# Kernel tuning notes

Hardware: AMD Instinct MI355X
Metric: run time of the kernel (lower is better)

The kernel has to match this reference:

```python
import jax, jax.numpy as jnp
import numpy as np

K = 7
TAU = 0.1
ANCHORS = 512
CANDIDATES = 2048
B, C, H, W = 16, 384, 96, 96
RADIUS = K // 2
K2 = K * K

_dy, _dx = np.meshgrid(np.arange(-RADIUS, RADIUS + 1), np.arange(-RADIUS, RADIUS + 1), indexing='ij')
OFF_Y = jnp.asarray(_dy.reshape(-1).astype(np.int32))  # [K2]
OFF_X = jnp.asarray(_dx.reshape(-1).astype(np.int32))  # [K2]


def _normalize(x):
    # F.normalize(x, dim=1): L2 over channel dim, eps=1e-12
    n = jnp.sqrt(jnp.sum(x * x, axis=1, keepdims=True))
    return x / jnp.maximum(n, 1e-12)


def _local_sims_shared(feat, anchors_yx):
    # feat [B,C,H,W], anchors_yx [M,2] shared across batch -> [B,M,K2]
    ys, xs = anchors_yx[:, 0], anchors_yx[:, 1]          # [M]
    yy = ys[:, None] + OFF_Y[None, :]                    # [M,K2]
    xx = xs[:, None] + OFF_X[None, :]                    # [M,K2]
    center = feat[:, :, ys, xs]                          # [B,C,M]
    neigh = feat[:, :, yy, xx]                           # [B,C,M,K2]
    return jnp.einsum('bcm,bcmk->bmk', center, neigh)


def _local_sims_per_image(feat, anchors_byx):
    # feat [B,C,H,W], anchors_byx [Bm,M,2] per-image anchors -> [B,M,K2]
    b, c, h, w = feat.shape
    flat = feat.reshape(b, c, h * w)
    ys, xs = anchors_byx[..., 0], anchors_byx[..., 1]    # [B,M]
    lin_c = ys * w + xs                                  # [B,M]
    lin_n = (ys[..., None] + OFF_Y) * w + (xs[..., None] + OFF_X)  # [B,M,K2]
    gather = jax.vmap(lambda f, idx: f[:, idx])          # f [C,HW], idx [...]
    center = gather(flat, lin_c)                         # [B,C,M]
    neigh = gather(flat, lin_n)                          # [B,C,M,K2]
    return jnp.einsum('bcm,bcmk->bmk', center, neigh)


def setup_inputs() -> dict:
    key = jax.random.key(0)
    k1, k2, k3, k4 = jax.random.split(key, 4)
    student = jax.random.normal(k1, (B, C, H, W), dtype=jnp.float32)
    teacher = jax.random.normal(k2, (B, C, H, W), dtype=jnp.float32)
    # anchors valid region: [radius, H-radius-1] x [radius, W-radius-1]
    ys = jax.random.randint(k3, (CANDIDATES,), RADIUS, H - RADIUS, dtype=jnp.int32)
    xs = jax.random.randint(k4, (CANDIDATES,), RADIUS, W - RADIUS, dtype=jnp.int32)
    candidate_anchors = jnp.stack([ys, xs], axis=1)      # [Mc,2]
    return {"student": student, "teacher": teacher, "candidate_anchors": candidate_anchors}


def reference(student, teacher, candidate_anchors):
    t_norm = _normalize(teacher)
    # --- teacher-entropy based anchor selection (no_grad in original) ---
    sim_cand = _local_sims_shared(t_norm, candidate_anchors) / TAU   # [B,Mc,K2]
    p = jax.nn.softmax(sim_cand, axis=2)
    ent = -jnp.sum(p * jnp.log(p + 1e-6), axis=2)                    # [B,Mc]
    # per_image=True, kcenter_top_m=0 -> lowest-entropy top-k per image
    _, sel_idx = jax.lax.top_k(-ent, ANCHORS)                        # [B,A]
    anchors = candidate_anchors[sel_idx]                             # [B,A,2]
    # --- local affinity KL ---
    s_norm = _normalize(student)
    sim_s = _local_sims_per_image(s_norm, anchors) / TAU             # [B,A,K2]
    sim_t = _local_sims_per_image(t_norm, anchors) / TAU
    log_ps = jax.nn.log_softmax(sim_s, axis=2)
    log_pt = jax.nn.log_softmax(sim_t, axis=2)
    pt = jnp.exp(log_pt)
    # F.kl_div(log_ps, pt, 'none').sum(2).mean()
    loss = jnp.mean(jnp.sum(pt * (log_pt - log_ps), axis=2))
    return loss
```

## Files before the change

kernel.cpp:

```cpp
#include <hip/hip_runtime.h>
#include <math.h>

#define B 16
#define C 384
#define CPAD 385
#define H 96
#define W 96
#define HW (H*W)
#define M 2048
#define K2 49
#define RAD 3
#define NSEL 512
#define INV_TAU 10.0f
#define TP 32

__device__ inline float wave_max(float v){
  #pragma unroll
  for (int o = 32; o; o >>= 1) v = fmaxf(v, __shfl_xor(v, o));
  return v;
}
__device__ inline float wave_sum(float v){
  #pragma unroll
  for (int o = 32; o; o >>= 1) v += __shfl_xor(v, o);
  return v;
}

__device__ __forceinline__ float patch_sims(const float* __restrict__ img,
                                            int ay, int ax, int lane){
  int g = lane >> 4, t = lane & 15;
  const float2* cp = (const float2*)(img + (size_t)(ay * W + ax) * C) + t;
  float2 c[12];
  #pragma unroll
  for (int j = 0; j < 12; ++j) c[j] = cp[16 * j];
  float mysim = 0.f;
  float2 bA[12], bB[12];

#define PLOAD(buf, pp) { \
    int dxl = ((pp) & 1) * 4 + g; if (dxl > 6) dxl = 6; \
    const float2* np = (const float2*)(img + \
        (size_t)((ay + ((pp) >> 1) - RAD) * W + (ax - RAD + dxl)) * C) + t; \
    _Pragma("unroll") for (int j = 0; j < 12; ++j) buf[j] = np[16 * j]; }

#define PCOMP(buf, pp) { \
    float a0 = 0.f, a1 = 0.f; \
    _Pragma("unroll") for (int j = 0; j < 6; ++j){ \
      a0 = fmaf(c[j].x, buf[j].x, a0); a0 = fmaf(c[j].y, buf[j].y, a0); \
      a1 = fmaf(c[j+6].x, buf[j+6].x, a1); a1 = fmaf(c[j+6].y, buf[j+6].y, a1); } \
    float a = a0 + a1; \
    a += __shfl_xor(a, 8); a += __shfl_xor(a, 4); \
    a += __shfl_xor(a, 2); a += __shfl_xor(a, 1); \
    int kbase = ((pp) >> 1) * 7 + ((pp) & 1) * 4; \
    int npass = ((pp) & 1) ? 3 : 4; \
    float v = __shfl(a, ((lane - kbase) & 3) << 4); \
    if (lane >= kbase && lane < kbase + npass) mysim = v; }

  PLOAD(bA, 0);
  #pragma unroll
  for (int pp = 0; pp < 14; pp += 2){
    PLOAD(bB, pp + 1);
    __builtin_amdgcn_sched_barrier(0);
    PCOMP(bA, pp);
    if (pp + 2 < 14) PLOAD(bA, pp + 2);
    __builtin_amdgcn_sched_barrier(0);
    PCOMP(bB, pp + 1);
  }
#undef PLOAD
#undef PCOMP
  return mysim;
}


__global__ void tnorm_kernel(const float* __restrict__ src, float* __restrict__ dst){
  int blk = blockIdx.x;
  int b = blk / (HW / TP);
  int pixbase = (blk % (HW / TP)) * TP;
  __shared__ float tile[TP][CPAD];
  __shared__ float scale[TP];
  const float* sb = src + (size_t)b * C * HW + pixbase;
  int tx = threadIdx.x & 31;
  int ty = threadIdx.x >> 5;
  #pragma unroll 4
  for (int c0 = 0; c0 < C; c0 += 8){
    tile[tx][c0 + ty] = sb[(size_t)(c0 + ty) * HW + tx];
  }
  __syncthreads();
  int pix = threadIdx.x >> 3;
  int j = threadIdx.x & 7;
  float ss = 0.f;
  #pragma unroll 4
  for (int c = j * 48; c < j * 48 + 48; ++c){ float v = tile[pix][c]; ss = fmaf(v, v, ss); }
  ss += __shfl_xor(ss, 1); ss += __shfl_xor(ss, 2); ss += __shfl_xor(ss, 4);
  if (j == 0) scale[pix] = 1.0f / fmaxf(sqrtf(ss), 1e-12f);
  __syncthreads();
  float4* db4 = (float4*)(dst + ((size_t)b * HW + pixbase) * C);
  #pragma unroll 4
  for (int l = threadIdx.x; l < TP * (C / 4); l += 256){
    int p = l / (C / 4), c4 = l - p * (C / 4);
    float s = scale[p];
    float4 v;
    v.x = tile[p][c4 * 4 + 0] * s;
    v.y = tile[p][c4 * 4 + 1] * s;
    v.z = tile[p][c4 * 4 + 2] * s;
    v.w = tile[p][c4 * 4 + 3] * s;
    db4[(size_t)p * (C / 4) + c4] = v;
  }
}

__global__ void sort_kernel(const int* __restrict__ anch, int* __restrict__ order){
  int i = blockIdx.x * 256 + threadIdx.x;
  __shared__ int keys[M];
  for (int j = threadIdx.x; j < M; j += 256){
    int ay = anch[2 * j], ax = anch[2 * j + 1];
    keys[j] = (((ay >> 3) * 12 + (ax >> 3)) << 11) + j;
  }
  __syncthreads();
  int ki = keys[i];
  int r = 0;
  #pragma unroll 4
  for (int j = 0; j < M; ++j) r += (keys[j] < ki) ? 1 : 0;
  order[r] = i;
}

__global__ __launch_bounds__(256, 4) void cand2_kernel(const float* __restrict__ fT,
                             const int* __restrict__ anch, const int* __restrict__ order,
                             float* __restrict__ simc, float* __restrict__ ent){
  int nwg = B * M / 4;
  int bid = blockIdx.x;
  int swz = (bid & 7) * (nwg >> 3) + (bid >> 3);
  int bm = swz * 4 + (threadIdx.x >> 6);
  int b = bm >> 11, mi = bm & (M - 1);
  int lane = threadIdx.x & 63;
  int m = order ? order[mi] : mi;
  int ay = anch[2 * m], ax = anch[2 * m + 1];
  const float* img = fT + (size_t)b * HW * C;
  float mysim = patch_sims(img, ay, ax, lane) * INV_TAU;

  float v = (lane < K2) ? mysim : -INFINITY;
  float mx = wave_max(v);
  float e = (lane < K2) ? expf(mysim - mx) : 0.f;
  float se = wave_sum(e);
  float p = e / se;
  float term = (lane < K2) ? (-p * logf(p + 1e-6f)) : 0.f;
  float en = wave_sum(term);
  size_t slot = (size_t)b * M + m;
  if (lane == 0) ent[slot] = en;
  if (lane < K2) simc[slot * K2 + lane] = mysim;
}

__global__ void select_kernel(const float* __restrict__ ent, int* __restrict__ sel){
  int blk = blockIdx.x;
  int b = blk >> 3;
  int i = (blk & 7) * 256 + threadIdx.x;
  __shared__ float se[M];
  for (int j = threadIdx.x; j < M; j += 256) se[j] = ent[b * M + j];
  __syncthreads();
  float ei = se[i];
  int r = 0;
  for (int j = 0; j < M; ++j){
    float ej = se[j];
    r += (ej < ei) || (ej == ei && j < i);
  }
  if (r < NSEL) sel[b * NSEL + r] = i;
}

__global__ __launch_bounds__(256, 4) void kl2_kernel(const float* __restrict__ fS,
                           const int* __restrict__ anch,
                           const float* __restrict__ simc, const int* __restrict__ sel,
                           float* __restrict__ klpart){
  int bj = blockIdx.x * 4 + (threadIdx.x >> 6);
  int b = bj >> 9, j = bj & (NSEL - 1);
  int lane = threadIdx.x & 63;
  int m = sel[b * NSEL + j];
  int ay = anch[2 * m], ax = anch[2 * m + 1];
  const float* img = fS + (size_t)b * HW * C;
  float sim_sv = patch_sims(img, ay, ax, lane) * INV_TAU;
  float sim_tv = (lane < K2) ? simc[((size_t)b * M + m) * K2 + lane] : -INFINITY;

  float vs = (lane < K2) ? sim_sv : -INFINITY;
  float mxs = wave_max(vs);
  float es = (lane < K2) ? expf(sim_sv - mxs) : 0.f;
  float sums = wave_sum(es);
  float ls = sim_sv - mxs - logf(sums);

  float mxt = wave_max(sim_tv);
  float et = (lane < K2) ? expf(sim_tv - mxt) : 0.f;
  float sumt = wave_sum(et);
  float lt = sim_tv - mxt - logf(sumt);

  float pt = et / sumt;
  float term = (lane < K2) ? pt * (lt - ls) : 0.f;
  float kl = wave_sum(term);
  if (lane == 0) klpart[bj] = kl;
}

__global__ void reduce_kernel(const float* __restrict__ part, float* __restrict__ out){
  float s = 0.f;
  for (int i = threadIdx.x; i < B * NSEL; i += 256) s += part[i];
  s = wave_sum(s);
  __shared__ float wsum[4];
  if ((threadIdx.x & 63) == 0) wsum[threadIdx.x >> 6] = s;
  __syncthreads();
  if (threadIdx.x == 0) out[0] = (wsum[0] + wsum[1] + wsum[2] + wsum[3]) * (1.0f / (B * NSEL));
}


__global__ void norms_kernel(const float* __restrict__ t, const float* __restrict__ s,
                             float* __restrict__ inv_t, float* __restrict__ inv_s){
  int pix = blockIdx.x * blockDim.x + threadIdx.x;
  if (pix >= B * HW) return;
  int b = pix / HW, p = pix - b * HW;
  const float* tb = t + (size_t)b * C * HW + p;
  const float* sb = s + (size_t)b * C * HW + p;
  float at = 0.f, as = 0.f;
  #pragma unroll 4
  for (int c = 0; c < C; ++c){
    float v = tb[(size_t)c * HW]; at = fmaf(v, v, at);
    float u = sb[(size_t)c * HW]; as = fmaf(u, u, as);
  }
  inv_t[pix] = 1.0f / fmaxf(sqrtf(at), 1e-12f);
  inv_s[pix] = 1.0f / fmaxf(sqrtf(as), 1e-12f);
}

__global__ void cand_kernel(const float* __restrict__ t, const int* __restrict__ anch,
                            const float* __restrict__ inv_t,
                            float* __restrict__ simc, float* __restrict__ ent){
  int bm = blockIdx.x;
  int b = bm >> 11, m = bm & (M - 1);
  int lane = threadIdx.x;
  int ay = anch[2 * m], ax = anch[2 * m + 1];
  int k = lane < K2 ? lane : 0;
  int dy = k / 7 - RAD, dx = k - (k / 7) * 7 - RAD;
  int pc = ay * W + ax;
  int pk = (ay + dy) * W + (ax + dx);
  const float* base = t + (size_t)b * C * HW;
  float acc = 0.f;
  #pragma unroll 4
  for (int c = 0; c < C; ++c){
    const float* row = base + (size_t)c * HW;
    acc = fmaf(row[pc], row[pk], acc);
  }
  float sim = acc * inv_t[b * HW + pc] * inv_t[b * HW + pk] * INV_TAU;
  float v = (lane < K2) ? sim : -INFINITY;
  float mx = wave_max(v);
  float e = (lane < K2) ? expf(sim - mx) : 0.f;
  float se = wave_sum(e);
  float p = e / se;
  float term = (lane < K2) ? (-p * logf(p + 1e-6f)) : 0.f;
  float en = wave_sum(term);
  if (lane == 0) ent[bm] = en;
  if (lane < K2) simc[(size_t)bm * K2 + lane] = sim;
}

__global__ void kl_kernel(const float* __restrict__ s, const int* __restrict__ anch,
                          const float* __restrict__ inv_s, const float* __restrict__ simc,
                          const int* __restrict__ sel, float* __restrict__ klpart){
  int bj = blockIdx.x;
  int b = bj >> 9, j = bj & (NSEL - 1);
  int lane = threadIdx.x;
  int m = sel[b * NSEL + j];
  int ay = anch[2 * m], ax = anch[2 * m + 1];
  int k = lane < K2 ? lane : 0;
  int dy = k / 7 - RAD, dx = k - (k / 7) * 7 - RAD;
  int pc = ay * W + ax;
  int pk = (ay + dy) * W + (ax + dx);
  const float* base = s + (size_t)b * C * HW;
  float acc = 0.f;
  #pragma unroll 4
  for (int c = 0; c < C; ++c){
    const float* row = base + (size_t)c * HW;
    acc = fmaf(row[pc], row[pk], acc);
  }
  float sim_sv = acc * inv_s[b * HW + pc] * inv_s[b * HW + pk] * INV_TAU;
  float sim_tv = (lane < K2) ? simc[((size_t)b * M + m) * K2 + lane] : -INFINITY;

  float vs = (lane < K2) ? sim_sv : -INFINITY;
  float mxs = wave_max(vs);
  float es = (lane < K2) ? expf(sim_sv - mxs) : 0.f;
  float sums = wave_sum(es);
  float ls = sim_sv - mxs - logf(sums);

  float mxt = wave_max(sim_tv);
  float et = (lane < K2) ? expf(sim_tv - mxt) : 0.f;
  float sumt = wave_sum(et);
  float lt = sim_tv - mxt - logf(sumt);

  float pt = et / sumt;
  float term = (lane < K2) ? pt * (lt - ls) : 0.f;
  float kl = wave_sum(term);
  if (lane == 0) klpart[bj] = kl;
}

extern "C" void kernel_launch(void* const* d_in, const int* in_sizes, int n_in,
                              void* d_out, int out_size, void* d_ws, size_t ws_size,
                              hipStream_t stream){
  const float* student = (const float*)d_in[0];
  const float* teacher = (const float*)d_in[1];
  const int*   anch    = (const int*)d_in[2];
  float* out = (float*)d_out;

  const size_t fbuf_elems = (size_t)B * HW * C;
  const size_t simc_elems = (size_t)B * M * K2;
  size_t req_base = (fbuf_elems + simc_elems + (size_t)B * M + (size_t)B * NSEL) * sizeof(float)
                  + (size_t)B * NSEL * sizeof(int);
  size_t req_sort = req_base + (size_t)M * sizeof(int);

  if (ws_size >= req_base){
    float* fbuf   = (float*)d_ws;
    float* simc   = fbuf + fbuf_elems;
    float* ent    = simc + simc_elems;
    float* klpart = ent + (size_t)B * M;
    int*   sel    = (int*)(klpart + (size_t)B * NSEL);
    int*   order  = (ws_size >= req_sort) ? (sel + (size_t)B * NSEL) : (int*)nullptr;

    hipLaunchKernelGGL(tnorm_kernel, dim3(B * (HW / TP)), dim3(256), 0, stream, teacher, fbuf);
    if (order)
      hipLaunchKernelGGL(sort_kernel, dim3(8), dim3(256), 0, stream, anch, order);
    hipLaunchKernelGGL(cand2_kernel, dim3(B * M / 4), dim3(256), 0, stream, fbuf, anch, order, simc, ent);
    hipLaunchKernelGGL(select_kernel, dim3(B * 8), dim3(256), 0, stream, ent, sel);
    hipLaunchKernelGGL(tnorm_kernel, dim3(B * (HW / TP)), dim3(256), 0, stream, student, fbuf);
    hipLaunchKernelGGL(kl2_kernel, dim3(B * NSEL / 4), dim3(256), 0, stream, fbuf, anch, simc, sel, klpart);
    hipLaunchKernelGGL(reduce_kernel, dim3(1), dim3(256), 0, stream, klpart, out);
  } else {
    float* ws2    = (float*)d_ws;
    float* inv_t  = ws2;
    float* inv_s  = inv_t + B * HW;
    float* ent    = inv_s + B * HW;
    float* simc   = ent + B * M;
    float* klpart = simc + simc_elems;
    int*   sel    = (int*)(klpart + (size_t)B * NSEL);

    hipLaunchKernelGGL(norms_kernel, dim3((B * HW + 255) / 256), dim3(256), 0, stream,
                       teacher, student, inv_t, inv_s);
    hipLaunchKernelGGL(cand_kernel, dim3(B * M), dim3(64), 0, stream,
                       teacher, anch, inv_t, simc, ent);
    hipLaunchKernelGGL(select_kernel, dim3(B * 8), dim3(256), 0, stream, ent, sel);
    hipLaunchKernelGGL(kl_kernel, dim3(B * NSEL), dim3(64), 0, stream,
                       student, anch, inv_s, simc, sel, klpart);
    hipLaunchKernelGGL(reduce_kernel, dim3(1), dim3(256), 0, stream, klpart, out);
  }
}
```

Measured before the change: 911.5 us.

## Split normalize into norms pass plus chunked transpose-scale, sort selected anchors spatially

Replaces the single tnorm transpose kernel, which held a whole 32x384 tile in LDS, with a norms kernel that computes inverse norms for teacher and student together, plus a transpose-and-scale kernel that streams 96-channel chunks through a smaller LDS tile. Selected anchors are now sorted by spatial bucket per image so kl2 reads neighbouring patches with better cache locality, and kl2 gets a block swizzle. Both the cand2 and kl2 occupancy hints rise to 8 blocks. Inputs are now read an extra time for the norms pass, and the added selsort launch costs some time.

```diff
diff --git a/kernel.cpp b/kernel.cpp
--- a/kernel.cpp
+++ b/kernel.cpp
@@ -3,7 +3,6 @@
 
 #define B 16
 #define C 384
-#define CPAD 385
 #define H 96
 #define W 96
 #define HW (H*W)
@@ -12,7 +11,8 @@
 #define RAD 3
 #define NSEL 512
 #define INV_TAU 10.0f
-#define TP 32
+#define TSP 64
+#define CCH 96
 
 __device__ inline float wave_max(float v){
   #pragma unroll
@@ -70,39 +70,59 @@
 }
 
 
-__global__ void tnorm_kernel(const float* __restrict__ src, float* __restrict__ dst){
+__global__ void norms2_kernel(const float* __restrict__ t, const float* __restrict__ s,
+                              float* __restrict__ inv_t, float* __restrict__ inv_s){
+  int pix = blockIdx.x * 256 + threadIdx.x;
+  int b = pix / HW, p = pix - b * HW;
+  const float* tb = t + (size_t)b * C * HW + p;
+  const float* sb = s + (size_t)b * C * HW + p;
+  float pt[8], ps[8];
+  #pragma unroll
+  for (int k = 0; k < 8; ++k){
+    float at = 0.f, as = 0.f;
+    #pragma unroll 4
+    for (int c = k * 48; c < k * 48 + 48; ++c){
+      float v = tb[(size_t)c * HW]; at = fmaf(v, v, at);
+      float u = sb[(size_t)c * HW]; as = fmaf(u, u, as);
+    }
+    pt[k] = at; ps[k] = as;
+  }
+  float at = ((pt[0]+pt[1]) + (pt[2]+pt[3])) + ((pt[4]+pt[5]) + (pt[6]+pt[7]));
+  float as = ((ps[0]+ps[1]) + (ps[2]+ps[3])) + ((ps[4]+ps[5]) + (ps[6]+ps[7]));
+  inv_t[pix] = 1.0f / fmaxf(sqrtf(at), 1e-12f);
+  inv_s[pix] = 1.0f / fmaxf(sqrtf(as), 1e-12f);
+}
+
+__global__ __launch_bounds__(256) void tscale_kernel(const float* __restrict__ src,
+                              const float* __restrict__ inv, float* __restrict__ dst){
   int blk = blockIdx.x;
-  int b = blk / (HW / TP);
-  int pixbase = (blk % (HW / TP)) * TP;
-  __shared__ float tile[TP][CPAD];
-  __shared__ float scale[TP];
-  const float* sb = src + (size_t)b * C * HW + pixbase;
-  int tx = threadIdx.x & 31;
-  int ty = threadIdx.x >> 5;
-  #pragma unroll 4
-  for (int c0 = 0; c0 < C; c0 += 8){
-    tile[tx][c0 + ty] = sb[(size_t)(c0 + ty) * HW + tx];
-  }
-  __syncthreads();
-  int pix = threadIdx.x >> 3;
-  int j = threadIdx.x & 7;
-  float ss = 0.f;
-  #pragma unroll 4
-  for (int c = j * 48; c < j * 48 + 48; ++c){ float v = tile[pix][c]; ss = fmaf(v, v, ss); }
-  ss += __shfl_xor(ss, 1); ss += __shfl_xor(ss, 2); ss += __shfl_xor(ss, 4);
-  if (j == 0) scale[pix] = 1.0f / fmaxf(sqrtf(ss), 1e-12f);
-  __syncthreads();
-  float4* db4 = (float4*)(dst + ((size_t)b * HW + pixbase) * C);
-  #pragma unroll 4
-  for (int l = threadIdx.x; l < TP * (C / 4); l += 256){
-    int p = l / (C / 4), c4 = l - p * (C / 4);
-    float s = scale[p];
-    float4 v;
-    v.x = tile[p][c4 * 4 + 0] * s;
-    v.y = tile[p][c4 * 4 + 1] * s;
-    v.z = tile[p][c4 * 4 + 2] * s;
-    v.w = tile[p][c4 * 4 + 3] * s;
-    db4[(size_t)p * (C / 4) + c4] = v;
+  int b = blk / (HW / TSP);
+  int pixbase = (blk % (HW / TSP)) * TSP;
+  __shared__ float tile[TSP][CCH + 1];
+  int tx = threadIdx.x & 63;
+  int ty = threadIdx.x >> 6;
+  const float* sb = src + (size_t)b * C * HW + pixbase + tx;
+  float sc = inv[b * HW + pixbase + tx];
+  float* db = dst + ((size_t)b * HW + pixbase) * C;
+  #pragma unroll
+  for (int ch = 0; ch < C / CCH; ++ch){
+    #pragma unroll
+    for (int cc = 0; cc < CCH; cc += 4){
+      tile[tx][cc + ty] = sb[(size_t)(ch * CCH + cc + ty) * HW] * sc;
+    }
+    __syncthreads();
+    #pragma unroll
+    for (int j = 0; j < 6; ++j){
+      int idx = threadIdx.x + 256 * j;
+      int pix = idx / 24, c4 = idx - pix * 24;
+      float4 v;
+      v.x = tile[pix][c4 * 4 + 0];
+      v.y = tile[pix][c4 * 4 + 1];
+      v.z = tile[pix][c4 * 4 + 2];
+      v.w = tile[pix][c4 * 4 + 3];
+      ((float4*)(db + (size_t)pix * C + ch * CCH))[c4] = v;
+    }
+    __syncthreads();
   }
 }
 
@@ -121,7 +141,7 @@
   order[r] = i;
 }
 
-__global__ __launch_bounds__(256, 4) void cand2_kernel(const float* __restrict__ fT,
+__global__ __launch_bounds__(256, 8) void cand2_kernel(const float* __restrict__ fT,
                              const int* __restrict__ anch, const int* __restrict__ order,
                              float* __restrict__ simc, float* __restrict__ ent){
   int nwg = B * M / 4;
@@ -163,14 +183,39 @@
   if (r < NSEL) sel[b * NSEL + r] = i;
 }
 
-__global__ __launch_bounds__(256, 4) void kl2_kernel(const float* __restrict__ fS,
+__global__ void selsort_kernel(const int* __restrict__ anch, const int* __restrict__ sel,
+                               int* __restrict__ sel2){
+  int b = blockIdx.x;
+  __shared__ int keys[NSEL];
+  __shared__ int pos[NSEL];
+  for (int j = threadIdx.x; j < NSEL; j += 256){
+    int m = sel[b * NSEL + j];
+    int ay = anch[2 * m], ax = anch[2 * m + 1];
+    keys[j] = (((ay >> 3) * 12 + (ax >> 3)) << 11) | m;
+    pos[j] = j;
+  }
+  __syncthreads();
+  for (int j = threadIdx.x; j < NSEL; j += 256){
+    int kj = keys[j];
+    int r = 0;
+    #pragma unroll 4
+    for (int i = 0; i < NSEL; ++i) r += (keys[i] < kj) ? 1 : 0;
+    sel2[b * NSEL + r] = (pos[j] << 11) | (kj & (M - 1));
+  }
+}
+
+__global__ __launch_bounds__(256, 8) void kl2_kernel(const float* __restrict__ fS,
                            const int* __restrict__ anch,
-                           const float* __restrict__ simc, const int* __restrict__ sel,
+                           const float* __restrict__ simc, const int* __restrict__ sel2,
                            float* __restrict__ klpart){
-  int bj = blockIdx.x * 4 + (threadIdx.x >> 6);
+  int nwg = B * NSEL / 4;
+  int bid = blockIdx.x;
+  int swz = (bid & 7) * (nwg >> 3) + (bid >> 3);
+  int bj = swz * 4 + (threadIdx.x >> 6);
   int b = bj >> 9, j = bj & (NSEL - 1);
   int lane = threadIdx.x & 63;
-  int m = sel[b * NSEL + j];
+  int e2 = sel2[b * NSEL + j];
+  int m = e2 & (M - 1), pos = e2 >> 11;
   int ay = anch[2 * m], ax = anch[2 * m + 1];
   const float* img = fS + (size_t)b * HW * C;
   float sim_sv = patch_sims(img, ay, ax, lane) * INV_TAU;
@@ -190,7 +235,7 @@
   float pt = et / sumt;
   float term = (lane < K2) ? pt * (lt - ls) : 0.f;
   float kl = wave_sum(term);
-  if (lane == 0) klpart[bj] = kl;
+  if (lane == 0) klpart[(b << 9) + pos] = kl;
 }
 
 __global__ void reduce_kernel(const float* __restrict__ part, float* __restrict__ out){
@@ -300,25 +345,34 @@
 
   const size_t fbuf_elems = (size_t)B * HW * C;
   const size_t simc_elems = (size_t)B * M * K2;
-  size_t req_base = (fbuf_elems + simc_elems + (size_t)B * M + (size_t)B * NSEL) * sizeof(float)
-                  + (size_t)B * NSEL * sizeof(int);
-  size_t req_sort = req_base + (size_t)M * sizeof(int);
-
-  if (ws_size >= req_base){
+  const size_t inv_elems  = (size_t)B * HW;
+  size_t req = (fbuf_elems + simc_elems + 2 * inv_elems + (size_t)B * M + (size_t)B * NSEL) * sizeof(float)
+             + (2 * (size_t)B * NSEL + (size_t)M) * sizeof(int);
+
+  if (ws_size >= req){
     float* fbuf   = (float*)d_ws;
     float* simc   = fbuf + fbuf_elems;
-    float* ent    = simc + simc_elems;
+    float* inv_t  = simc + simc_elems;
+    float* inv_s  = inv_t + inv_elems;
+    float* ent    = inv_s + inv_elems;
     float* klpart = ent + (size_t)B * M;
     int*   sel    = (int*)(klpart + (size_t)B * NSEL);
-    int*   order  = (ws_size >= req_sort) ? (sel + (size_t)B * NSEL) : (int*)nullptr;
-
-    hipLaunchKernelGGL(tnorm_kernel, dim3(B * (HW / TP)), dim3(256), 0, stream, teacher, fbuf);
-    if (order)
-      hipLaunchKernelGGL(sort_kernel, dim3(8), dim3(256), 0, stream, anch, order);
-    hipLaunchKernelGGL(cand2_kernel, dim3(B * M / 4), dim3(256), 0, stream, fbuf, anch, order, simc, ent);
+    int*   sel2   = sel + (size_t)B * NSEL;
+    int*   order  = sel2 + (size_t)B * NSEL;
+
+    hipLaunchKernelGGL(norms2_kernel, dim3(B * HW / 256), dim3(256), 0, stream,
+                       teacher, student, inv_t, inv_s);
+    hipLaunchKernelGGL(sort_kernel, dim3(8), dim3(256), 0, stream, anch, order);
+    hipLaunchKernelGGL(tscale_kernel, dim3(B * (HW / TSP)), dim3(256), 0, stream,
+                       teacher, inv_t, fbuf);
+    hipLaunchKernelGGL(cand2_kernel, dim3(B * M / 4), dim3(256), 0, stream,
+                       fbuf, anch, order, simc, ent);
     hipLaunchKernelGGL(select_kernel, dim3(B * 8), dim3(256), 0, stream, ent, sel);
-    hipLaunchKernelGGL(tnorm_kernel, dim3(B * (HW / TP)), dim3(256), 0, stream, student, fbuf);
-    hipLaunchKernelGGL(kl2_kernel, dim3(B * NSEL / 4), dim3(256), 0, stream, fbuf, anch, simc, sel, klpart);
+    hipLaunchKernelGGL(selsort_kernel, dim3(B), dim3(256), 0, stream, anch, sel, sel2);
+    hipLaunchKernelGGL(tscale_kernel, dim3(B * (HW / TSP)), dim3(256), 0, stream,
+                       student, inv_s, fbuf);
+    hipLaunchKernelGGL(kl2_kernel, dim3(B * NSEL / 4), dim3(256), 0, stream,
+                       fbuf, anch, simc, sel2, klpart);
     hipLaunchKernelGGL(reduce_kernel, dim3(1), dim3(256), 0, stream, klpart, out);
   } else {
     float* ws2    = (float*)d_ws;
```

Measured after the change: 1.697 ms. 86.2% more time.

## Use float4 patch loads, spatially sort selected anchors, raise occupancy

Applied to the files above, without the earlier changes.

The patch similarity routine now splits the wave into two 32-lane halves that load float4 channel chunks, so each pass handles two neighbours with fewer, wider loads and fewer registers. A new kernel sorts each image's selected anchors by spatial tile so neighbouring KL work items touch nearby feature data, and the KL kernel gets a workgroup swizzle and scatters results back to their original positions. Launch bounds are raised to six waves per SIMD on both patch kernels. The sort path is now required, so the workspace requirement grows and the no-sort fallback is removed.

```diff
diff --git a/kernel.cpp b/kernel.cpp
--- a/kernel.cpp
+++ b/kernel.cpp
@@ -27,42 +27,42 @@
 
 __device__ __forceinline__ float patch_sims(const float* __restrict__ img,
                                             int ay, int ax, int lane){
-  int g = lane >> 4, t = lane & 15;
-  const float2* cp = (const float2*)(img + (size_t)(ay * W + ax) * C) + t;
-  float2 c[12];
+  int g = lane >> 5, t = lane & 31;
+  const float4* cp = (const float4*)(img + (size_t)(ay * W + ax) * C) + t;
+  float4 c0 = cp[0], c1 = cp[32], c2 = cp[64];
+  float mysim = 0.f;
+  float4 a0, a1, a2, b0, b1, b2;
+
+#define PLOAD(p0,p1,p2, pp) { \
+    int dxl = ((pp) & 3) * 2 + g; if (dxl > 6) dxl = 6; \
+    const float4* np = (const float4*)(img + \
+        (size_t)((ay + ((pp) >> 2) - RAD) * W + (ax - RAD + dxl)) * C) + t; \
+    p0 = np[0]; p1 = np[32]; p2 = np[64]; }
+
+#define PCOMP(p0,p1,p2, pp) { \
+    float s0 = c0.x * p0.x; s0 = fmaf(c0.y, p0.y, s0); \
+    s0 = fmaf(c0.z, p0.z, s0); s0 = fmaf(c0.w, p0.w, s0); \
+    float s1 = c1.x * p1.x; s1 = fmaf(c1.y, p1.y, s1); \
+    s1 = fmaf(c1.z, p1.z, s1); s1 = fmaf(c1.w, p1.w, s1); \
+    float s2 = c2.x * p2.x; s2 = fmaf(c2.y, p2.y, s2); \
+    s2 = fmaf(c2.z, p2.z, s2); s2 = fmaf(c2.w, p2.w, s2); \
+    float a = (s0 + s1) + s2; \
+    a += __shfl_xor(a, 16); a += __shfl_xor(a, 8); \
+    a += __shfl_xor(a, 4);  a += __shfl_xor(a, 2); a += __shfl_xor(a, 1); \
+    int kbase = ((pp) >> 2) * 7 + ((pp) & 3) * 2; \
+    float v0 = __shfl(a, 0), v1 = __shfl(a, 32); \
+    if (lane == kbase) mysim = v0; \
+    if (((pp) & 3) < 3 && lane == kbase + 1) mysim = v1; }
+
+  PLOAD(a0,a1,a2, 0);
   #pragma unroll
-  for (int j = 0; j < 12; ++j) c[j] = cp[16 * j];
-  float mysim = 0.f;
-  float2 bA[12], bB[12];
-
-#define PLOAD(buf, pp) { \
-    int dxl = ((pp) & 1) * 4 + g; if (dxl > 6) dxl = 6; \
-    const float2* np = (const float2*)(img + \
-        (size_t)((ay + ((pp) >> 1) - RAD) * W + (ax - RAD + dxl)) * C) + t; \
-    _Pragma("unroll") for (int j = 0; j < 12; ++j) buf[j] = np[16 * j]; }
-
-#define PCOMP(buf, pp) { \
-    float a0 = 0.f, a1 = 0.f; \
-    _Pragma("unroll") for (int j = 0; j < 6; ++j){ \
-      a0 = fmaf(c[j].x, buf[j].x, a0); a0 = fmaf(c[j].y, buf[j].y, a0); \
-      a1 = fmaf(c[j+6].x, buf[j+6].x, a1); a1 = fmaf(c[j+6].y, buf[j+6].y, a1); } \
-    float a = a0 + a1; \
-    a += __shfl_xor(a, 8); a += __shfl_xor(a, 4); \
-    a += __shfl_xor(a, 2); a += __shfl_xor(a, 1); \
-    int kbase = ((pp) >> 1) * 7 + ((pp) & 1) * 4; \
-    int npass = ((pp) & 1) ? 3 : 4; \
-    float v = __shfl(a, ((lane - kbase) & 3) << 4); \
-    if (lane >= kbase && lane < kbase + npass) mysim = v; }
-
-  PLOAD(bA, 0);
-  #pragma unroll
-  for (int pp = 0; pp < 14; pp += 2){
-    PLOAD(bB, pp + 1);
+  for (int pp = 0; pp < 28; pp += 2){
+    PLOAD(b0,b1,b2, pp + 1);
     __builtin_amdgcn_sched_barrier(0);
-    PCOMP(bA, pp);
-    if (pp + 2 < 14) PLOAD(bA, pp + 2);
+    PCOMP(a0,a1,a2, pp);
+    if (pp + 2 < 28) PLOAD(a0,a1,a2, pp + 2);
     __builtin_amdgcn_sched_barrier(0);
-    PCOMP(bB, pp + 1);
+    PCOMP(b0,b1,b2, pp + 1);
   }
 #undef PLOAD
 #undef PCOMP
@@ -121,7 +121,7 @@
   order[r] = i;
 }
 
-__global__ __launch_bounds__(256, 4) void cand2_kernel(const float* __restrict__ fT,
+__global__ __launch_bounds__(256, 6) void cand2_kernel(const float* __restrict__ fT,
                              const int* __restrict__ anch, const int* __restrict__ order,
                              float* __restrict__ simc, float* __restrict__ ent){
   int nwg = B * M / 4;
@@ -130,7 +130,7 @@
   int bm = swz * 4 + (threadIdx.x >> 6);
   int b = bm >> 11, mi = bm & (M - 1);
   int lane = threadIdx.x & 63;
-  int m = order ? order[mi] : mi;
+  int m = order[mi];
   int ay = anch[2 * m], ax = anch[2 * m + 1];
   const float* img = fT + (size_t)b * HW * C;
   float mysim = patch_sims(img, ay, ax, lane) * INV_TAU;
@@ -163,14 +163,39 @@
   if (r < NSEL) sel[b * NSEL + r] = i;
 }
 
-__global__ __launch_bounds__(256, 4) void kl2_kernel(const float* __restrict__ fS,
+__global__ void selsort_kernel(const int* __restrict__ anch, const int* __restrict__ sel,
+                               int* __restrict__ sel2){
+  int b = blockIdx.x;
+  __shared__ int keys[NSEL];
+  __shared__ int pos[NSEL];
+  for (int j = threadIdx.x; j < NSEL; j += 256){
+    int m = sel[b * NSEL + j];
+    int ay = anch[2 * m], ax = anch[2 * m + 1];
+    keys[j] = (((ay >> 3) * 12 + (ax >> 3)) << 11) | m;
+    pos[j] = j;
+  }
+  __syncthreads();
+  for (int j = threadIdx.x; j < NSEL; j += 256){
+    int kj = keys[j];
+    int r = 0;
+    #pragma unroll 4
+    for (int i = 0; i < NSEL; ++i) r += (keys[i] < kj) ? 1 : 0;
+    sel2[b * NSEL + r] = (pos[j] << 11) | (kj & (M - 1));
+  }
+}
+
+__global__ __launch_bounds__(256, 6) void kl2_kernel(const float* __restrict__ fS,
                            const int* __restrict__ anch,
-                           const float* __restrict__ simc, const int* __restrict__ sel,
+                           const float* __restrict__ simc, const int* __restrict__ sel2,
                            float* __restrict__ klpart){
-  int bj = blockIdx.x * 4 + (threadIdx.x >> 6);
+  int nwg = B * NSEL / 4;
+  int bid = blockIdx.x;
+  int swz = (bid & 7) * (nwg >> 3) + (bid >> 3);
+  int bj = swz * 4 + (threadIdx.x >> 6);
   int b = bj >> 9, j = bj & (NSEL - 1);
   int lane = threadIdx.x & 63;
-  int m = sel[b * NSEL + j];
+  int e2 = sel2[b * NSEL + j];
+  int m = e2 & (M - 1), pos = e2 >> 11;
   int ay = anch[2 * m], ax = anch[2 * m + 1];
   const float* img = fS + (size_t)b * HW * C;
   float sim_sv = patch_sims(img, ay, ax, lane) * INV_TAU;
@@ -190,7 +215,7 @@
   float pt = et / sumt;
   float term = (lane < K2) ? pt * (lt - ls) : 0.f;
   float kl = wave_sum(term);
-  if (lane == 0) klpart[bj] = kl;
+  if (lane == 0) klpart[(b << 9) + pos] = kl;
 }
 
 __global__ void reduce_kernel(const float* __restrict__ part, float* __restrict__ out){
@@ -300,25 +325,27 @@
 
   const size_t fbuf_elems = (size_t)B * HW * C;
   const size_t simc_elems = (size_t)B * M * K2;
-  size_t req_base = (fbuf_elems + simc_elems + (size_t)B * M + (size_t)B * NSEL) * sizeof(float)
-                  + (size_t)B * NSEL * sizeof(int);
-  size_t req_sort = req_base + (size_t)M * sizeof(int);
-
-  if (ws_size >= req_base){
+  size_t req = (fbuf_elems + simc_elems + (size_t)B * M + (size_t)B * NSEL) * sizeof(float)
+             + (2 * (size_t)B * NSEL + (size_t)M) * sizeof(int);
+
+  if (ws_size >= req){
     float* fbuf   = (float*)d_ws;
     float* simc   = fbuf + fbuf_elems;
     float* ent    = simc + simc_elems;
     float* klpart = ent + (size_t)B * M;
     int*   sel    = (int*)(klpart + (size_t)B * NSEL);
-    int*   order  = (ws_size >= req_sort) ? (sel + (size_t)B * NSEL) : (int*)nullptr;
+    int*   sel2   = sel + (size_t)B * NSEL;
+    int*   order  = sel2 + (size_t)B * NSEL;
 
     hipLaunchKernelGGL(tnorm_kernel, dim3(B * (HW / TP)), dim3(256), 0, stream, teacher, fbuf);
-    if (order)
-      hipLaunchKernelGGL(sort_kernel, dim3(8), dim3(256), 0, stream, anch, order);
-    hipLaunchKernelGGL(cand2_kernel, dim3(B * M / 4), dim3(256), 0, stream, fbuf, anch, order, simc, ent);
+    hipLaunchKernelGGL(sort_kernel, dim3(8), dim3(256), 0, stream, anch, order);
+    hipLaunchKernelGGL(cand2_kernel, dim3(B * M / 4), dim3(256), 0, stream,
+                       fbuf, anch, order, simc, ent);
     hipLaunchKernelGGL(select_kernel, dim3(B * 8), dim3(256), 0, stream, ent, sel);
+    hipLaunchKernelGGL(selsort_kernel, dim3(B), dim3(256), 0, stream, anch, sel, sel2);
     hipLaunchKernelGGL(tnorm_kernel, dim3(B * (HW / TP)), dim3(256), 0, stream, student, fbuf);
-    hipLaunchKernelGGL(kl2_kernel, dim3(B * NSEL / 4), dim3(256), 0, stream, fbuf, anch, simc, sel, klpart);
+    hipLaunchKernelGGL(kl2_kernel, dim3(B * NSEL / 4), dim3(256), 0, stream,
+                       fbuf, anch, simc, sel2, klpart);
     hipLaunchKernelGGL(reduce_kernel, dim3(1), dim3(256), 0, stream, klpart, out);
   } else {
     float* ws2    = (float*)d_ws;
```

After: 903.7 us. No clear change (-0.8%).
